# Kernel tuning notes

Hardware: AMD Instinct MI355X
Metric: run time of the kernel (lower is better)

## Reference

```python
import jax, jax.numpy as jnp
import numpy as np


def _refl_conv(x, w, b, pad, stride):
    # ReflectionPad2d(pad) followed by Conv2d(stride=stride), NCHW / OIHW layouts.
    x = jnp.pad(x, ((0, 0), (0, 0), (pad, pad), (pad, pad)), mode='reflect')
    y = jax.lax.conv_general_dilated(
        x, w, window_strides=(stride, stride), padding='VALID',
        dimension_numbers=('NCHW', 'OIHW', 'NCHW'))
    return y + b[None, :, None, None]


def setup_inputs() -> dict:
    key = jax.random.key(0)
    ks = jax.random.split(key, 16)
    B, C, H, W = 8, 128, 64, 64
    IH, IW = 4 * H, 4 * W
    g = 0.02  # init gain ('normal' init in source)
    f32 = jnp.float32
    return {
        'feature_in': jax.random.normal(ks[0], (B, C, H, W), f32),
        'imgs': jax.random.uniform(ks[1], (B, 3, IH, IW), dtype=f32),
        'masks': jax.random.uniform(ks[2], (B, 1, IH, IW), dtype=f32),
        # Gate conv stack params (torch OIHW layout), biases zero per init_weights
        'gw1': g * jax.random.normal(ks[3], (32, 4, 7, 7), f32),
        'gb1': jnp.zeros((32,), f32),
        'gw2': g * jax.random.normal(ks[4], (64, 32, 5, 5), f32),
        'gb2': jnp.zeros((64,), f32),
        'gw3': g * jax.random.normal(ks[5], (128, 64, 5, 5), f32),
        'gb3': jnp.zeros((128,), f32),
        'gw4': g * jax.random.normal(ks[6], (256, 128, 3, 3), f32),
        'gb4': jnp.zeros((256,), f32),
        'gw5': g * jax.random.normal(ks[7], (1, 256, 3, 3), f32),
        'gb5': jnp.zeros((1,), f32),
        # combiner: Conv2d(2C -> C, 1x1)
        'cw': g * jax.random.normal(ks[8], (C, 2 * C, 1, 1), f32),
        'cb': jnp.zeros((C,), f32),
    }


def reference(feature_in, imgs, masks, gw1, gb1, gw2, gb2, gw3, gb3,
              gw4, gb4, gw5, gb5, cw, cb):
    PI = 3.1415926
    # ---- Gate ----
    x = jnp.concatenate([imgs, masks], axis=1)          # [B,4,4H,4W]
    s = jax.nn.relu(_refl_conv(x, gw1, gb1, 3, 1))
    s = jax.nn.relu(_refl_conv(s, gw2, gb2, 2, 2))
    s = jax.nn.relu(_refl_conv(s, gw3, gb3, 2, 1))
    s = jax.nn.relu(_refl_conv(s, gw4, gb4, 1, 2))
    s = jax.nn.relu(_refl_conv(s, gw5, gb5, 1, 1))      # [B,1,H,W]
    s = jnp.tan(PI * (jnp.tanh(s) - 0.5))
    B, C, H, W = feature_in.shape
    P = H * W
    gate = s.reshape(B, P, 1, 1)                        # row-major pixel order
    # ---- Att (patch_size=1: kernels are per-pixel feature vectors) ----
    K = feature_in.reshape(B, C, P).transpose(0, 2, 1) + 1e-7   # [B,P,C]
    Kn = K / jnp.sqrt(jnp.sum(K * K, axis=-1, keepdims=True))
    # attention_scores = conv2d(feature_map, K_norm) == cosine-like similarity
    scores = jnp.einsum('bpc,bcyx->bpyx', Kn, feature_in) + gate  # [B,P,H,W]
    A = jax.nn.softmax(scores, axis=1)
    # conv_transpose2d with 1x1 kernels == weighted sum of (unnormalized) kernels
    att = jnp.einsum('bpyx,bpc->bcyx', A, K)            # [B,C,H,W]
    # ---- combiner (1x1 conv on concat) ----
    cat = jnp.concatenate([att, feature_in], axis=1)    # [B,2C,H,W]
    out = jnp.einsum('oc,bcyx->boyx', cw[:, :, 0, 0], cat) + cb[None, :, None, None]
    return out
```

## Files before the change

kernel.cpp:

```cpp
#include <hip/hip_runtime.h>
#include <hip/hip_bf16.h>
#include <hip/hip_fp16.h>
#include <math.h>


#define PI_F 3.1415926f

typedef __attribute__((ext_vector_type(8))) short short8;
typedef __attribute__((ext_vector_type(4))) float f32x4;
typedef _Float16 half8 __attribute__((ext_vector_type(8)));
typedef __attribute__((ext_vector_type(4))) unsigned short u16x4;
typedef unsigned short ushort_t;

__device__ __forceinline__ ushort_t f2bf(float x) {
    unsigned u = __float_as_uint(x);
    unsigned r = (u + 0x7FFFu + ((u >> 16) & 1u)) >> 16;
    return (ushort_t)r;
}
__device__ __forceinline__ void split16(float x, ushort_t& h, ushort_t& l) {
    __half hh = __float2half(x);
    h = __half_as_ushort(hh);
    l = __half_as_ushort(__float2half(x - __half2float(hh)));
}
__device__ __forceinline__ ushort_t f2h(float x) {
    return __half_as_ushort(__float2half(x));
}
__device__ __forceinline__ int swz(int r, int c) {
    return ((c ^ r ^ (r >> 2)) & 3) << 3;
}

__global__ __launch_bounds__(256) void transform_w_k(
    const float* __restrict__ w, ushort_t* __restrict__ Wh, ushort_t* __restrict__ Wl,
    int Cout, int Cin, int KK)
{
    int idx = blockIdx.x * 256 + threadIdx.x;
    int N = Cout * Cin * KK;
    if (idx >= N) return;
    int oc = idx / (Cin * KK);
    int rem = idx - oc * (Cin * KK);
    int ic = rem / KK;
    int t = rem - ic * KK;
    float v = w[idx];
    long dst = ((long)t * Cout + oc) * Cin + ic;
    split16(v, Wh[dst], Wl[dst]);
}

__global__ __launch_bounds__(256) void transform_w1_k(
    const float* __restrict__ w, ushort_t* __restrict__ Wh, ushort_t* __restrict__ Wl)
{
    int idx = blockIdx.x * 256 + threadIdx.x;
    if (idx >= 7 * 32 * 32) return;
    int ky = idx / 1024;
    int rem = idx - ky * 1024;
    int oc = rem >> 5;
    int k = rem & 31;
    float v = 0.f;
    if (k < 28) {
        int kx = k >> 2, ic = k & 3;
        v = w[((oc * 4 + ic) * 7 + ky) * 7 + kx];
    }
    split16(v, Wh[idx], Wl[idx]);
}

__global__ __launch_bounds__(256) void prep_in_k(
    const float* __restrict__ imgs, const float* __restrict__ masks,
    ushort_t* __restrict__ Xh)
{
    const int iy = blockIdx.x, b = blockIdx.y;
    int sy = iy - 3; if (sy < 0) sy = -sy; if (sy >= 256) sy = 510 - sy;
    const int rb = sy << 8;
    const float* i0 = imgs + (long)b * 3 * 65536;
    const float* mk = masks + (long)b * 65536;
    for (int x = threadIdx.x; x < 262; x += 256) {
        int sx = x - 3; if (sx < 0) sx = -sx; if (sx >= 256) sx = 510 - sx;
        u16x4 hv;
        hv[0] = f2h(i0[rb + sx]);
        hv[1] = f2h(i0[65536 + rb + sx]);
        hv[2] = f2h(i0[131072 + rb + sx]);
        hv[3] = f2h(mk[rb + sx]);
        long o = ((long)(b * 262 + iy) * 262 + x) * 4;
        *(u16x4*)&Xh[o] = hv;
    }
}

__global__ __launch_bounds__(256) void conv1_mfma_k(
    const ushort_t* __restrict__ Xinh,
    const ushort_t* __restrict__ W1h, const ushort_t* __restrict__ W1l,
    const float* __restrict__ bias, ushort_t* __restrict__ Oh)
{
    const int tid = threadIdx.x, lane = tid & 63, wid = tid >> 6;
    const int wm = wid & 1, wn = wid >> 1, l15 = lane & 15, quad = lane >> 4;
    const int ox0 = blockIdx.x * 64;
    const int oy = blockIdx.y, b = blockIdx.z;
    f32x4 acc[2];
    acc[0] = (f32x4){0.f, 0.f, 0.f, 0.f};
    acc[1] = (f32x4){0.f, 0.f, 0.f, 0.f};
#pragma unroll
    for (int ky = 0; ky < 7; ++ky) {
        long wo = (long)(ky * 32 + wm * 16 + l15) * 32 + quad * 8;
        half8 Ah = *(const half8*)&W1h[wo];
        half8 Al = *(const half8*)&W1l[wo];
        long xrow = ((long)(b * 262 + oy + ky) * 262 + ox0) * 4;
#pragma unroll
        for (int ni = 0; ni < 2; ++ni) {
            long xo = xrow + (wn * 32 + ni * 16 + l15) * 4 + quad * 8;
            half8 Bh = *(const half8*)&Xinh[xo];
            acc[ni] = __builtin_amdgcn_mfma_f32_16x16x32_f16(Ah, Bh, acc[ni], 0, 0, 0);
            acc[ni] = __builtin_amdgcn_mfma_f32_16x16x32_f16(Al, Bh, acc[ni], 0, 0, 0);
        }
    }
    const int ocf = wm * 16 + quad * 4;
    float4 bv = *(const float4*)&bias[ocf];
#pragma unroll
    for (int ni = 0; ni < 2; ++ni) {
        int n = ox0 + wn * 32 + ni * 16 + l15;
        u16x4 hv;
        hv[0] = f2h(fmaxf(acc[ni][0] + bv.x, 0.f));
        hv[1] = f2h(fmaxf(acc[ni][1] + bv.y, 0.f));
        hv[2] = f2h(fmaxf(acc[ni][2] + bv.z, 0.f));
        hv[3] = f2h(fmaxf(acc[ni][3] + bv.w, 0.f));
        long o = ((long)(b * 260 + oy + 2) * 260 + n + 2) * 32 + ocf;
        *(u16x4*)&Oh[o] = hv;
    }
}

__global__ __launch_bounds__(256) void pad_cl_k(
    ushort_t* __restrict__ Xh, int Hp, int Wp, int PAD, int C, int H, int W)
{
    const int iy = blockIdx.x, b = blockIdx.y;
    int t = iy - PAD; if (t < 0) t = -t; if (t >= H) t = 2 * H - 2 - t;
    const int iys = t + PAD;
    const long rowd = ((long)(b * Hp + iy) * Wp) * C;
    const long rows = ((long)(b * Hp + iys) * Wp) * C;
    const int nch = Wp * (C >> 3);
    for (int idx = threadIdx.x; idx < nch; idx += 256) {
        int x = idx / (C >> 3);
        int cg = (idx - x * (C >> 3)) << 3;
        int t2 = x - PAD; if (t2 < 0) t2 = -t2; if (t2 >= W) t2 = 2 * W - 2 - t2;
        int xs = t2 + PAD;
        if (xs == x && iys == iy) continue;
        *(int4*)&Xh[rowd + (long)x * C + cg] = *(const int4*)&Xh[rows + (long)xs * C + cg];
    }
}

template<int K, int S, int CIN, int CSTG, int MT, int NPX, bool WRITE_CL>
__global__ __launch_bounds__(256, 2) void conv_mfma_k(
    const ushort_t* __restrict__ Xh,
    const ushort_t* __restrict__ Wh, const ushort_t* __restrict__ Wl,
    const float* __restrict__ bias,
    int Hp, int Wp, int CoutT,
    ushort_t* __restrict__ Oh, int Hpn, int Wpn, int NP,
    float* __restrict__ Ofp)
{
    constexpr int WS = (NPX - 1) * S + K;
    constexpr int WS2 = (WS + 1) / 2;
    constexpr int MF = MT / 32;
    constexpr int NF = NPX / 32;
    __shared__ ushort_t Bsh[WS * CSTG];
    __shared__ ushort_t Ash[K * MT * CSTG];
    __shared__ ushort_t Asl[K * MT * CSTG];
    const int tid = threadIdx.x, lane = tid & 63, wid = tid >> 6;
    const int wm = wid & 1, wn = wid >> 1, l15 = lane & 15, quad = lane >> 4;
    const int bx = blockIdx.x, oy = blockIdx.y;
    const int NOC = CoutT / MT;
    const int ocg = blockIdx.z % NOC, b = blockIdx.z / NOC;
    const int ox0 = bx * NPX;

    f32x4 acc[MF][NF];
#pragma unroll
    for (int mi = 0; mi < MF; ++mi)
#pragma unroll
        for (int ni = 0; ni < NF; ++ni) acc[mi][ni] = (f32x4){0.f, 0.f, 0.f, 0.f};

#pragma unroll
    for (int ky = 0; ky < K; ++ky) {
        const long rowoff = ((long)(b * Hp + oy * S + ky) * Wp + ox0 * S) * CIN;
        for (int cs = 0; cs < CIN; cs += CSTG) {
            __syncthreads();
            constexpr int NCH = WS * CSTG / 8;
#pragma unroll
            for (int it = 0; it < (NCH + 255) / 256; ++it) {
                int flat = tid + it * 256;
                if (flat < NCH) {
                    int e0 = flat * 8;
                    int x = e0 / CSTG;
                    int cpos = (e0 - x * CSTG) >> 3;
                    int xs = (S == 1) ? x : ((x >> 1) + (x & 1) * WS2);
                    *(int4*)&Bsh[xs * CSTG + swz(xs, cpos)] =
                        *(const int4*)&Xh[rowoff + (long)x * CIN + cs + cpos * 8];
                }
            }
            constexpr int NW = K * MT * CSTG / 8;
#pragma unroll
            for (int it = 0; it < (NW + 255) / 256; ++it) {
                int flat = tid + it * 256;
                if (flat < NW) {
                    int e0 = flat * 8;
                    int kx = e0 / (MT * CSTG);
                    int rem = e0 - kx * MT * CSTG;
                    int oc = rem / CSTG;
                    int cpos = (rem - oc * CSTG) >> 3;
                    int arow = kx * MT + oc;
                    int dst = arow * CSTG + swz(arow, cpos);
                    long src = ((long)((ky * K + kx) * CoutT + ocg * MT + oc)) * CIN + cs + cpos * 8;
                    *(int4*)&Ash[dst] = *(const int4*)&Wh[src];
                    *(int4*)&Asl[dst] = *(const int4*)&Wl[src];
                }
            }
            __syncthreads();
#pragma unroll
            for (int kx = 0; kx < K; ++kx) {
                half8 Ah[MF], Al[MF], Bh[NF];
#pragma unroll
                for (int mi = 0; mi < MF; ++mi) {
                    int arow = kx * MT + wm * (MT / 2) + mi * 16 + l15;
                    int ao = arow * CSTG + swz(arow, quad);
                    Ah[mi] = *(const half8*)&Ash[ao];
                    Al[mi] = *(const half8*)&Asl[ao];
                }
#pragma unroll
                for (int ni = 0; ni < NF; ++ni) {
                    int m = wn * (NPX / 2) + ni * 16 + l15;
                    int xs = (S == 1) ? (m + kx) : (m + (kx >> 1) + (kx & 1) * WS2);
                    Bh[ni] = *(const half8*)&Bsh[xs * CSTG + swz(xs, quad)];
                }
#pragma unroll
                for (int mi = 0; mi < MF; ++mi)
#pragma unroll
                    for (int ni = 0; ni < NF; ++ni) {
                        acc[mi][ni] = __builtin_amdgcn_mfma_f32_16x16x32_f16(Ah[mi], Bh[ni], acc[mi][ni], 0, 0, 0);
                        acc[mi][ni] = __builtin_amdgcn_mfma_f32_16x16x32_f16(Al[mi], Bh[ni], acc[mi][ni], 0, 0, 0);
                    }
            }
        }
    }
#pragma unroll
    for (int ni = 0; ni < NF; ++ni) {
        const int n = ox0 + wn * (NPX / 2) + ni * 16 + l15;
#pragma unroll
        for (int mi = 0; mi < MF; ++mi) {
            const int ocf = ocg * MT + wm * (MT / 2) + mi * 16 + quad * 4;
            float4 bv = *(const float4*)&bias[ocf];
            float v0 = fmaxf(acc[mi][ni][0] + bv.x, 0.f);
            float v1 = fmaxf(acc[mi][ni][1] + bv.y, 0.f);
            float v2 = fmaxf(acc[mi][ni][2] + bv.z, 0.f);
            float v3 = fmaxf(acc[mi][ni][3] + bv.w, 0.f);
            if (WRITE_CL) {
                long o = ((long)(b * Hpn + oy + NP) * Wpn + n + NP) * CoutT + ocf;
                u16x4 hv;
                hv[0] = f2h(v0); hv[1] = f2h(v1); hv[2] = f2h(v2); hv[3] = f2h(v3);
                *(u16x4*)&Oh[o] = hv;
            } else {
                long o = ((long)(b * CoutT + ocf) << 12) + (oy << 6) + n;
                Ofp[o] = v0;
                Ofp[o + 4096] = v1;
                Ofp[o + 8192] = v2;
                Ofp[o + 12288] = v3;
            }
        }
    }
}

__global__ __launch_bounds__(256) void conv5_gate_k(
    const float* __restrict__ s4, const float* __restrict__ w,
    const float* __restrict__ bias, float* __restrict__ gate)
{
    const int tid = threadIdx.x;
    const int lane = tid & 63, g = tid >> 6;
    const int oy = blockIdx.x, b = blockIdx.y;
    int ixo[3], iyo[3];
#pragma unroll
    for (int k = 0; k < 3; ++k) {
        int ix = lane + k - 1; if (ix < 0) ix = -ix; if (ix >= 64) ix = 126 - ix;
        int iy = oy + k - 1; if (iy < 0) iy = -iy; if (iy >= 64) iy = 126 - iy;
        ixo[k] = ix; iyo[k] = iy << 6;
    }
    float part = 0.f;
    const float* inb = s4 + ((long)b * 256 + g * 64) * 4096;
    const float* wg = w + g * 64 * 9;
    for (int ic = 0; ic < 64; ++ic) {
        const float* inc = inb + ic * 4096;
        const float* wc = wg + ic * 9;
#pragma unroll
        for (int ky = 0; ky < 3; ++ky)
#pragma unroll
            for (int kx = 0; kx < 3; ++kx)
                part = fmaf(wc[ky * 3 + kx], inc[iyo[ky] + ixo[kx]], part);
    }
    __shared__ float red[4][64];
    red[g][lane] = part;
    __syncthreads();
    if (tid < 64) {
        float s = bias[0] + red[0][tid] + red[1][tid] + red[2][tid] + red[3][tid];
        s = fmaxf(s, 0.f);
        gate[(b << 12) + (oy << 6) + tid] = tanf(PI_F * (tanhf(s) - 0.5f));
    }
}

__global__ __launch_bounds__(256) void invn_k(const float* __restrict__ F, float* __restrict__ invn)
{
    const int p = blockIdx.x * 256 + threadIdx.x;
    const int b = blockIdx.y;
    const float* Fb = F + (long)b * 524288;
    float ss = 0.f;
#pragma unroll 8
    for (int c = 0; c < 128; ++c) {
        float v = Fb[c * 4096 + p] + 1e-7f;
        ss = fmaf(v, v, ss);
    }
    invn[(b << 12) + p] = 1.0f / sqrtf(ss);
}

__global__ __launch_bounds__(256) void prep_bf16_k(
    const float* __restrict__ F, ushort_t* __restrict__ Vf,
    ushort_t* __restrict__ Fa, ushort_t* __restrict__ Ft16)
{
    __shared__ float Ls[128][65];
    const int tid = threadIdx.x;
    const int lane = tid & 63, wv = tid >> 6;
    const int p0 = blockIdx.x * 64, b = blockIdx.y;
#pragma unroll 8
    for (int cc = 0; cc < 32; ++cc) {
        int c = wv * 32 + cc;
        long idx = ((long)b * 128 + c) * 4096 + p0 + lane;
        Ls[c][lane] = F[idx];
    }
    __syncthreads();
#pragma unroll 8
    for (int i = 0; i < 32; ++i) {
        int flat = tid + 256 * i;
        int c = flat & 127, pl_ = flat >> 7;
        Ft16[((long)b * 4096 + p0 + pl_) * 128 + c] = f2bf(Ls[c][pl_]);
    }
    const int chunk0 = blockIdx.x * 2;
#pragma unroll
    for (int s = tid; s < 1024; s += 256) {
        int ck = s >> 9, rem = s & 511;
        int ct = rem >> 6, ln = rem & 63;
        int c = ct * 16 + (ln & 15);
        int pl = ck * 32 + (ln >> 4) * 8;
        ushort_t tmp[8];
#pragma unroll
        for (int e = 0; e < 8; ++e) tmp[e] = f2bf(Ls[c][pl + e]);
        *(short8*)&Vf[(((long)(b * 128 + chunk0 + ck) * 8 + ct) * 64 + ln) * 8] = *(short8*)tmp;
    }
#pragma unroll
    for (int s = tid; s < 1024; s += 256) {
        int ck = s >> 9, rem = s & 511;
        int f = rem >> 6, ln = rem & 63;
        int l15_ = ln & 15;
        int c0 = (f & 3) * 32 + (ln >> 4) * 8;
        int pl = ck * 32 + ((l15_ & 12) << 1) + (l15_ & 3) + (f >> 2) * 4;
        ushort_t tmp[8];
#pragma unroll
        for (int e = 0; e < 8; ++e) tmp[e] = f2bf(Ls[c0 + e][pl]);
        *(short8*)&Fa[(((long)(b * 128 + chunk0 + ck) * 8 + f) * 64 + ln) * 8] = *(short8*)tmp;
    }
}

__global__ __launch_bounds__(64, 1) void flash_attn_k(
    const ushort_t* __restrict__ Ft16, const ushort_t* __restrict__ Vf,
    const ushort_t* __restrict__ Fa,
    const float* __restrict__ invn, const float* __restrict__ gate,
    float* __restrict__ Opart, float* __restrict__ lpart)
{
    const int lane = threadIdx.x & 63;
    const int l15 = lane & 15, quad = lane >> 4;
    const int b = blockIdx.x;
    const int qb = blockIdx.y & 63, ks = blockIdx.y >> 6;
    const int q0 = qb * 64;
    const int bp = b << 12;
    const ushort_t* Ftb = Ft16 + (long)b * 4096 * 128;
    const ushort_t* FaB = Fa + (long)b * 128 * 8 * 512;
    const ushort_t* VfB = Vf + (long)b * 128 * 8 * 512;

    short8 Bq[4][4];
#pragma unroll
    for (int ni = 0; ni < 4; ++ni)
#pragma unroll
        for (int cs = 0; cs < 4; ++cs)
            Bq[ni][cs] = *(const short8*)&Ftb[(long)(q0 + ni * 16 + l15) * 128 + cs * 32 + quad * 8];

    f32x4 O[8][4];
#pragma unroll
    for (int ct = 0; ct < 8; ++ct)
#pragma unroll
        for (int ni = 0; ni < 4; ++ni) O[ct][ni] = (f32x4){0.f, 0.f, 0.f, 0.f};
    float l_acc[4] = {0.f, 0.f, 0.f, 0.f};

    union BeU { short8 v; __hip_bfloat162 h[4]; };
    const int p_beg = ks * 1024;
    const int ck_beg = ks * 32;
    const long lane8 = (long)lane * 8;

    short8 Ap[2][2][4];
    short8 Va[2][8];
    float4 ivb[2][2], gtb[2][2];

    {
        const long fb = (long)(ck_beg) * 4096;
#pragma unroll
        for (int sub = 0; sub < 2; ++sub) {
#pragma unroll
            for (int cs = 0; cs < 4; ++cs)
                Ap[0][sub][cs] = *(const short8*)&FaB[fb + (long)(sub * 4 + cs) * 512 + lane8];
            ivb[0][sub] = *(const float4*)&invn[bp + p_beg + quad * 8 + sub * 4];
            gtb[0][sub] = *(const float4*)&gate[bp + p_beg + quad * 8 + sub * 4];
        }
#pragma unroll
        for (int ct = 0; ct < 8; ++ct)
            Va[0][ct] = *(const short8*)&VfB[fb + (long)ct * 512 + lane8];
    }

#pragma unroll 2
    for (int t = 0; t < 32; ++t) {
        const int cur = t & 1, nxt = cur ^ 1;
        if (t + 1 < 32) {
            const int p1 = p_beg + (t + 1) * 32;
            const long fb = (long)(ck_beg + t + 1) * 4096;
#pragma unroll
            for (int sub = 0; sub < 2; ++sub) {
#pragma unroll
                for (int cs = 0; cs < 4; ++cs)
                    Ap[nxt][sub][cs] = *(const short8*)&FaB[fb + (long)(sub * 4 + cs) * 512 + lane8];
                ivb[nxt][sub] = *(const float4*)&invn[bp + p1 + quad * 8 + sub * 4];
                gtb[nxt][sub] = *(const float4*)&gate[bp + p1 + quad * 8 + sub * 4];
            }
#pragma unroll
            for (int ct = 0; ct < 8; ++ct)
                Va[nxt][ct] = *(const short8*)&VfB[fb + (long)ct * 512 + lane8];
        }
        BeU be[4];
#pragma unroll
        for (int sub = 0; sub < 2; ++sub) {
            f32x4 Sa[4];
#pragma unroll
            for (int ni = 0; ni < 4; ++ni) Sa[ni] = (f32x4){0.f, 0.f, 0.f, 0.f};
#pragma unroll
            for (int cs = 0; cs < 4; ++cs)
#pragma unroll
                for (int ni = 0; ni < 4; ++ni)
                    Sa[ni] = __builtin_amdgcn_mfma_f32_16x16x32_bf16(Ap[cur][sub][cs], Bq[ni][cs], Sa[ni], 0, 0, 0);
            const float4 iv = ivb[cur][sub];
            const float4 gt = gtb[cur][sub];
#pragma unroll
            for (int ni = 0; ni < 4; ++ni) {
                float e0 = __expf(fmaf(Sa[ni][0], iv.x, gt.x));
                float e1 = __expf(fmaf(Sa[ni][1], iv.y, gt.y));
                float e2 = __expf(fmaf(Sa[ni][2], iv.z, gt.z));
                float e3 = __expf(fmaf(Sa[ni][3], iv.w, gt.w));
                be[ni].h[sub * 2]     = __float22bfloat162_rn(make_float2(e0, e1));
                be[ni].h[sub * 2 + 1] = __float22bfloat162_rn(make_float2(e2, e3));
                l_acc[ni] += (e0 + e1) + (e2 + e3);
            }
        }
#pragma unroll
        for (int ct = 0; ct < 8; ++ct)
#pragma unroll
            for (int ni = 0; ni < 4; ++ni)
                O[ct][ni] = __builtin_amdgcn_mfma_f32_16x16x32_bf16(Va[cur][ct], be[ni].v, O[ct][ni], 0, 0, 0);
    }

#pragma unroll
    for (int ni = 0; ni < 4; ++ni) {
        float lt = l_acc[ni];
        lt += __shfl_xor(lt, 16);
        lt += __shfl_xor(lt, 32);
        if (quad == 0)
            lpart[(ks * 8 + b) * 4096 + q0 + ni * 16 + l15] = lt;
    }
    float* Ob = Opart + (long)(ks * 8 + b) * 524288;
#pragma unroll
    for (int ct = 0; ct < 8; ++ct)
#pragma unroll
        for (int ni = 0; ni < 4; ++ni) {
            int c = ct * 16 + quad * 4;
            int q = q0 + ni * 16 + l15;
#pragma unroll
            for (int r = 0; r < 4; ++r)
                Ob[((long)(c + r) << 12) + q] = O[ct][ni][r];
        }
}

__global__ __launch_bounds__(256) void combiner_k(
    const float* __restrict__ Opart, const float* __restrict__ lpart,
    const float* __restrict__ F, const float* __restrict__ cw,
    const float* __restrict__ cb, float* __restrict__ out)
{
    const int tid = threadIdx.x;
    const int q = blockIdx.x * 256 + tid;
    const int o0 = blockIdx.y << 4;
    const int b = blockIdx.z;
    float lsum = 0.f;
#pragma unroll
    for (int ks = 0; ks < 4; ++ks) lsum += lpart[(ks * 8 + b) * 4096 + q];
    float il = 1.0f / lsum;
    const float* Fb = F + (long)b * 524288 + q;
    float acc[16];
#pragma unroll
    for (int j = 0; j < 16; ++j) acc[j] = cb[o0 + j];
    for (int c = 0; c < 128; ++c) {
        float a = 0.f;
#pragma unroll
        for (int ks = 0; ks < 4; ++ks)
            a += Opart[(long)(ks * 8 + b) * 524288 + (long)c * 4096 + q];
        a *= il;
        float f = Fb[(long)c * 4096];
#pragma unroll
        for (int j = 0; j < 16; ++j) {
            acc[j] = fmaf(cw[(o0 + j) * 256 + c], a, acc[j]);
            acc[j] = fmaf(cw[(o0 + j) * 256 + 128 + c], f, acc[j]);
        }
    }
#pragma unroll
    for (int j = 0; j < 16; ++j)
        out[((long)(b * 128 + o0 + j) << 12) + q] = acc[j];
}

extern "C" void kernel_launch(void* const* d_in, const int* in_sizes, int n_in,
                              void* d_out, int out_size, void* d_ws, size_t ws_size,
                              hipStream_t stream)
{
    const float* F     = (const float*)d_in[0];
    const float* imgs  = (const float*)d_in[1];
    const float* masks = (const float*)d_in[2];
    const float* gw1 = (const float*)d_in[3];  const float* gb1 = (const float*)d_in[4];
    const float* gw2 = (const float*)d_in[5];  const float* gb2 = (const float*)d_in[6];
    const float* gw3 = (const float*)d_in[7];  const float* gb3 = (const float*)d_in[8];
    const float* gw4 = (const float*)d_in[9];  const float* gb4 = (const float*)d_in[10];
    const float* gw5 = (const float*)d_in[11]; const float* gb5 = (const float*)d_in[12];
    const float* cw  = (const float*)d_in[13]; const float* cb  = (const float*)d_in[14];
    float* out = (float*)d_out;

    float* W = (float*)d_ws;
    ushort_t* Xcl2h = (ushort_t*)(W);
    ushort_t* Xcl4h = (ushort_t*)(W);
    float*    Opart = W;
    float*    lpart = W + 16777216;
    ushort_t* Xcl3h = (ushort_t*)(W + 17305600);
    ushort_t* Vf    = (ushort_t*)(W + 17305600);
    float*    s4   = W + 26226688;
    ushort_t* Fa   = (ushort_t*)(W + 26226688);
    ushort_t* Ft16 = (ushort_t*)(W + 30420992);
    ushort_t* W2h = (ushort_t*)(W + 34615296);
    ushort_t* W2l = (ushort_t*)(W + 34640896);
    ushort_t* W3h = (ushort_t*)(W + 34666496);
    ushort_t* W3l = (ushort_t*)(W + 34768896);
    ushort_t* W4h = (ushort_t*)(W + 34871296);
    ushort_t* W4l = (ushort_t*)(W + 35018752);
    float* gate = W + 35166208;
    float* invn = W + 35198976;
    ushort_t* Xinh = (ushort_t*)(W + 35231744);
    ushort_t* W1h  = (ushort_t*)(W + 37428416);
    ushort_t* W1l  = (ushort_t*)(W + 37432000);

    transform_w_k<<<dim3(200),  256, 0, stream>>>(gw2, W2h, W2l, 64, 32, 25);
    transform_w_k<<<dim3(800),  256, 0, stream>>>(gw3, W3h, W3l, 128, 64, 25);
    transform_w_k<<<dim3(1152), 256, 0, stream>>>(gw4, W4h, W4l, 256, 128, 9);
    transform_w1_k<<<dim3(28), 256, 0, stream>>>(gw1, W1h, W1l);
    prep_in_k<<<dim3(262, 8), 256, 0, stream>>>(imgs, masks, Xinh);

    conv1_mfma_k<<<dim3(4, 256, 8), 256, 0, stream>>>(Xinh, W1h, W1l, gb1, Xcl2h);
    pad_cl_k<<<dim3(260, 8), 256, 0, stream>>>(Xcl2h, 260, 260, 2, 32, 256, 256);
    conv_mfma_k<5, 2, 32, 32, 64, 128, true><<<dim3(1, 128, 8), 256, 0, stream>>>(
        Xcl2h, W2h, W2l, gb2, 260, 260, 64, Xcl3h, 132, 132, 2, nullptr);
    pad_cl_k<<<dim3(132, 8), 256, 0, stream>>>(Xcl3h, 132, 132, 2, 64, 128, 128);
    conv_mfma_k<5, 1, 64, 32, 64, 128, true><<<dim3(1, 128, 16), 256, 0, stream>>>(
        Xcl3h, W3h, W3l, gb3, 132, 132, 128, Xcl4h, 130, 130, 1, nullptr);
    pad_cl_k<<<dim3(130, 8), 256, 0, stream>>>(Xcl4h, 130, 130, 1, 128, 128, 128);
    conv_mfma_k<3, 2, 128, 32, 128, 64, false><<<dim3(1, 64, 16), 256, 0, stream>>>(
        Xcl4h, W4h, W4l, gb4, 130, 130, 256, nullptr, 0, 0, 0, s4);
    conv5_gate_k<<<dim3(64, 8), 256, 0, stream>>>(s4, gw5, gb5, gate);

    invn_k<<<dim3(16, 8), 256, 0, stream>>>(F, invn);
    prep_bf16_k<<<dim3(64, 8), 256, 0, stream>>>(F, Vf, Fa, Ft16);
    flash_attn_k<<<dim3(8, 256, 1), 64, 0, stream>>>(Ft16, Vf, Fa, invn, gate, Opart, lpart);
    combiner_k<<<dim3(16, 8, 8), 256, 0, stream>>>(Opart, lpart, F, cw, cb, out);
}
```

Baseline: 594.3 us.

## Add specialized conv3 kernel computing four output rows per block with rolling input-row buffer

```diff
diff --git a/kernel.cpp b/kernel.cpp
--- a/kernel.cpp
+++ b/kernel.cpp
@@ -256,6 +256,117 @@
                 Ofp[o + 4096] = v1;
                 Ofp[o + 8192] = v2;
                 Ofp[o + 12288] = v3;
+            }
+        }
+    }
+}
+
+__global__ __launch_bounds__(256, 2) void conv3_mfma_k(
+    const ushort_t* __restrict__ Xh,
+    const ushort_t* __restrict__ Wh, const ushort_t* __restrict__ Wl,
+    const float* __restrict__ bias, ushort_t* __restrict__ Oh)
+{
+    __shared__ ushort_t Bsh[4][132 * 32];
+    __shared__ ushort_t Ash[5 * 64 * 32];
+    __shared__ ushort_t Asl[5 * 64 * 32];
+    const int tid = threadIdx.x, lane = tid & 63, wid = tid >> 6;
+    const int wm = wid & 1, wn = wid >> 1, l15 = lane & 15, quad = lane >> 4;
+    const int oy0 = blockIdx.y * 4;
+    const int ocg = blockIdx.z & 1, b = blockIdx.z >> 1;
+
+    f32x4 acc[4][2][4];
+#pragma unroll
+    for (int oyi = 0; oyi < 4; ++oyi)
+#pragma unroll
+        for (int mi = 0; mi < 2; ++mi)
+#pragma unroll
+            for (int ni = 0; ni < 4; ++ni) acc[oyi][mi][ni] = (f32x4){0.f, 0.f, 0.f, 0.f};
+
+    for (int csi = 0; csi < 2; ++csi) {
+        const int cb = csi * 32;
+        for (int flat = tid; flat < 3 * 528; flat += 256) {
+            int r0 = flat / 528;
+            int rem = flat - r0 * 528;
+            int e0 = rem * 8;
+            int x = e0 >> 5;
+            int cpos = (e0 & 31) >> 3;
+            *(int4*)&Bsh[r0][x * 32 + swz(x, cpos)] =
+                *(const int4*)&Xh[((long)(b * 132 + oy0 + r0) * 132 + x) * 64 + cb + cpos * 8];
+        }
+        for (int ky = 0; ky < 5; ++ky) {
+            {
+                const int row = oy0 + ky + 3;
+                const int slot = (ky + 3) & 3;
+                for (int flat = tid; flat < 528; flat += 256) {
+                    int e0 = flat * 8;
+                    int x = e0 >> 5;
+                    int cpos = (e0 & 31) >> 3;
+                    *(int4*)&Bsh[slot][x * 32 + swz(x, cpos)] =
+                        *(const int4*)&Xh[((long)(b * 132 + row) * 132 + x) * 64 + cb + cpos * 8];
+                }
+            }
+            for (int flat = tid; flat < 1280; flat += 256) {
+                int e0 = flat * 8;
+                int kx = e0 >> 11;
+                int rem = e0 & 2047;
+                int oc = rem >> 5;
+                int cpos = (rem & 31) >> 3;
+                int arow = kx * 64 + oc;
+                int dst = arow * 32 + swz(arow, cpos);
+                long src = ((long)((ky * 5 + kx) * 128 + ocg * 64 + oc)) * 64 + cb + cpos * 8;
+                *(int4*)&Ash[dst] = *(const int4*)&Wh[src];
+                *(int4*)&Asl[dst] = *(const int4*)&Wl[src];
+            }
+            __syncthreads();
+#pragma unroll
+            for (int kx = 0; kx < 5; ++kx) {
+                half8 Ah[2], Al[2];
+#pragma unroll
+                for (int mi = 0; mi < 2; ++mi) {
+                    int arow = kx * 64 + wm * 32 + mi * 16 + l15;
+                    int ao = arow * 32 + swz(arow, quad);
+                    Ah[mi] = *(const half8*)&Ash[ao];
+                    Al[mi] = *(const half8*)&Asl[ao];
+                }
+#pragma unroll
+                for (int oyi = 0; oyi < 4; ++oyi) {
+                    const int slot = (ky + oyi) & 3;
+                    half8 Bh[4];
+#pragma unroll
+                    for (int ni = 0; ni < 4; ++ni) {
+                        int xs = wn * 64 + ni * 16 + l15 + kx;
+                        Bh[ni] = *(const half8*)&Bsh[slot][xs * 32 + swz(xs, quad)];
+                    }
+#pragma unroll
+                    for (int mi = 0; mi < 2; ++mi)
+#pragma unroll
+                        for (int ni = 0; ni < 4; ++ni) {
+                            acc[oyi][mi][ni] = __builtin_amdgcn_mfma_f32_16x16x32_f16(Ah[mi], Bh[ni], acc[oyi][mi][ni], 0, 0, 0);
+                            acc[oyi][mi][ni] = __builtin_amdgcn_mfma_f32_16x16x32_f16(Al[mi], Bh[ni], acc[oyi][mi][ni], 0, 0, 0);
+                        }
+                }
+            }
+            __syncthreads();
+        }
+    }
+    const int ocf = ocg * 64 + wm * 32 + quad * 4;
+#pragma unroll
+    for (int oyi = 0; oyi < 4; ++oyi) {
+        const int oy = oy0 + oyi;
+#pragma unroll
+        for (int ni = 0; ni < 4; ++ni) {
+            const int n = wn * 64 + ni * 16 + l15;
+#pragma unroll
+            for (int mi = 0; mi < 2; ++mi) {
+                const int oc4 = ocf + mi * 16;
+                float4 bv = *(const float4*)&bias[oc4];
+                u16x4 hv;
+                hv[0] = f2h(fmaxf(acc[oyi][mi][ni][0] + bv.x, 0.f));
+                hv[1] = f2h(fmaxf(acc[oyi][mi][ni][1] + bv.y, 0.f));
+                hv[2] = f2h(fmaxf(acc[oyi][mi][ni][2] + bv.z, 0.f));
+                hv[3] = f2h(fmaxf(acc[oyi][mi][ni][3] + bv.w, 0.f));
+                long o = ((long)(b * 130 + oy + 1) * 130 + n + 1) * 128 + oc4;
+                *(u16x4*)&Oh[o] = hv;
             }
         }
     }
@@ -565,8 +676,7 @@
     conv_mfma_k<5, 2, 32, 32, 64, 128, true><<<dim3(1, 128, 8), 256, 0, stream>>>(
         Xcl2h, W2h, W2l, gb2, 260, 260, 64, Xcl3h, 132, 132, 2, nullptr);
     pad_cl_k<<<dim3(132, 8), 256, 0, stream>>>(Xcl3h, 132, 132, 2, 64, 128, 128);
-    conv_mfma_k<5, 1, 64, 32, 64, 128, true><<<dim3(1, 128, 16), 256, 0, stream>>>(
-        Xcl3h, W3h, W3l, gb3, 132, 132, 128, Xcl4h, 130, 130, 1, nullptr);
+    conv3_mfma_k<<<dim3(1, 32, 16), 256, 0, stream>>>(Xcl3h, W3h, W3l, gb3, Xcl4h);
     pad_cl_k<<<dim3(130, 8), 256, 0, stream>>>(Xcl4h, 130, 130, 1, 128, 128, 128);
     conv_mfma_k<3, 2, 128, 32, 128, 64, false><<<dim3(1, 64, 16), 256, 0, stream>>>(
         Xcl4h, W4h, W4l, gb4, 130, 130, 256, nullptr, 0, 0, 0, s4);
```

Result: faster. 561.9 us (-5.5%).
